# Optimization experiments

Measured on AMD Instinct MI355X. Metric: run time of the kernel, lower is better.

The kernel has to match this reference:

```python
import jax, jax.numpy as jnp
import numpy as np

D_MODEL = 1024
N_HEADS = 16
HEAD_DIM = D_MODEL // N_HEADS


def setup_inputs() -> dict:
    key = jax.random.key(0)
    k_x, k_qkv, k_proj = jax.random.split(key, 3)
    x = jax.random.normal(k_x, (2, 2048, D_MODEL), dtype=jnp.float32)
    # flax nnx.Linear kernels: shape (in_features, out_features), lecun_normal-ish scale
    w_qkv = jax.random.normal(k_qkv, (D_MODEL, 3 * D_MODEL), dtype=jnp.float32) / np.sqrt(D_MODEL)
    w_proj = jax.random.normal(k_proj, (D_MODEL, D_MODEL), dtype=jnp.float32) / np.sqrt(D_MODEL)
    return {"x": x, "w_qkv": w_qkv, "w_proj": w_proj}


def reference(x, w_qkv, w_proj):
    bsz, seq_len, d_model = x.shape
    qkv = x @ w_qkv  # (B, T, 3*D)
    q, k, v = jnp.split(qkv, 3, axis=-1)
    q = q.reshape(bsz, seq_len, N_HEADS, HEAD_DIM)
    k = k.reshape(bsz, seq_len, N_HEADS, HEAD_DIM)
    v = v.reshape(bsz, seq_len, N_HEADS, HEAD_DIM)
    scale = jnp.sqrt(jnp.asarray(HEAD_DIM, dtype=x.dtype))
    attn_logits = jnp.einsum('bthd,bshd->bhts', q / scale, k)  # (B, H, T, T)
    attn_weights = jax.nn.softmax(attn_logits, axis=-1)
    attn_out = jnp.einsum('bhts,bshd->bthd', attn_weights, v)
    attn_out = attn_out.reshape(bsz, seq_len, d_model)
    return attn_out @ w_proj
```

## Files before the change

kernel.cpp:

```cpp
#include <hip/hip_runtime.h>
#include <hip/hip_bf16.h>
#include <cmath>

#define D_MODEL 1024
#define NH 16
#define HD 64
#define BSZ 2
#define SEQ 2048
#define MTOT (BSZ * SEQ)

typedef _Float16 f16x8 __attribute__((ext_vector_type(8)));
typedef __fp16   fp16x2 __attribute__((ext_vector_type(2)));
typedef float    f32x4  __attribute__((ext_vector_type(4)));
typedef float    f32x16 __attribute__((ext_vector_type(16)));
typedef unsigned int uivec2 __attribute__((ext_vector_type(2)));

#define QSCALE 0.18033688011112042f

__device__ __forceinline__ ushort f2h(float x) {
    union { _Float16 h; ushort u; } cv;
    cv.h = (_Float16)x;
    return cv.u;
}
__device__ __forceinline__ uint pkh(float a, float b) {
    union { fp16x2 h; uint u; } cv;
    cv.h = __builtin_amdgcn_cvt_pkrtz(a, b);
    return cv.u;
}
__device__ __forceinline__ float fexp2(float x) {
    float r; asm("v_exp_f32 %0, %1" : "=v"(r) : "v"(x)); return r;
}
__device__ __forceinline__ float fmax3(float a, float b, float c) {
    return fmaxf(fmaxf(a, b), c);
}
__device__ __forceinline__ void gload_lds16(const ushort* g, ushort* l) {
    __builtin_amdgcn_global_load_lds(
        (const __attribute__((address_space(1))) void*)g,
        (__attribute__((address_space(3))) void*)l, 16, 0, 0);
}

__global__ __launch_bounds__(256)
void transpose_cast2(const float* __restrict__ A, const float* __restrict__ B,
                     ushort* __restrict__ At, ushort* __restrict__ Bt)
{
    __shared__ float tile[32][33];
    const int z = blockIdx.z;
    const float* in = (z < 3) ? A : B;
    ushort* out     = (z < 3) ? At : Bt;
    const int C     = (z < 3) ? 3 * D_MODEL : D_MODEL;
    const int cb    = (z < 3) ? z * 32 + blockIdx.x : blockIdx.x;
    const int R = D_MODEL;
    const int t  = threadIdx.x;
    const int r0 = blockIdx.y * 32, c0 = cb * 32;
    const int tr = t >> 5, tc = t & 31;
#pragma unroll
    for (int s = 0; s < 4; ++s)
        tile[tr + 8 * s][tc] = in[(size_t)(r0 + tr + 8 * s) * C + c0 + tc];
    __syncthreads();
#pragma unroll
    for (int s = 0; s < 4; ++s)
        out[(size_t)(c0 + tr + 8 * s) * R + r0 + tc] = f2h(tile[tc][tr + 8 * s]);
}

__global__ __launch_bounds__(256)
void gemm_qkv(const float* __restrict__ A, const ushort* __restrict__ Bt,
              ushort* __restrict__ Qw, ushort* __restrict__ Kw,
              ushort* __restrict__ Vw)
{
    __shared__ ushort As[3][128 * 32];
    __shared__ ushort Bs[3][128 * 32];

    const int t  = threadIdx.x;
    const int w  = t >> 6;
    const int l  = t & 63;
    const int lr = l & 15;
    const int lg = l >> 4;
    const int wr = w >> 1, wc = w & 1;

    const int gx   = gridDim.x;
    const int nwg  = gx * gridDim.y;
    const int lin  = blockIdx.y * gx + blockIdx.x;
    const int lin2 = (lin & 7) * (nwg >> 3) + (lin >> 3);
    const int m0   = (lin2 / gx) * 128;
    const int n0   = (lin2 % gx) * 128;

    const float*  Ab = A  + (size_t)m0 * 1024;
    const ushort* Bb = Bt + (size_t)n0 * 1024;

    f32x4 acc[4][4];
#pragma unroll
    for (int i = 0; i < 4; ++i)
#pragma unroll
        for (int j = 0; j < 4; ++j) acc[i][j] = (f32x4){0.f, 0.f, 0.f, 0.f};

    const int arow = w * 32 + (l >> 3);
    const int acol = (l & 7) * 4;
    float4 ar[4];
    auto loadA = [&](int kt) {
#pragma unroll
        for (int s = 0; s < 4; ++s)
            ar[s] = *(const float4*)(Ab + (size_t)(arow + s * 8) * 1024
                                        + kt * 32 + acol);
    };
    auto writeA = [&](int buf) {
#pragma unroll
        for (int s = 0; s < 4; ++s) {
            alignas(8) ushort e4[4];
            e4[0] = f2h(ar[s].x); e4[1] = f2h(ar[s].y);
            e4[2] = f2h(ar[s].z); e4[3] = f2h(ar[s].w);
            *(uint2*)&As[buf][(arow + s * 8) * 32 + acol] = *(const uint2*)e4;
        }
    };
    auto stageB = [&](int buf, int kt) {
#pragma unroll
        for (int s = 0; s < 2; ++s) {
            const int c    = s * 64 + l;
            const int row  = w * 32 + (c >> 2);
            const int unit = c & 3;
            gload_lds16(Bb + (size_t)row * 1024 + kt * 32 + unit * 8,
                        &Bs[buf][(w * 128 + s * 64) * 8]);
        }
    };

    auto body = [&](int kt, int cb, int vm) {
        if (vm == 2) asm volatile("s_waitcnt vmcnt(2)" ::: "memory");
        else         asm volatile("s_waitcnt vmcnt(0)" ::: "memory");
        asm volatile("s_waitcnt lgkmcnt(0)" ::: "memory");
        __builtin_amdgcn_s_barrier();

        if (kt + 1 < 32) writeA((cb + 1) % 3);
        if (kt + 2 < 32) { loadA(kt + 2); stageB((cb + 2) % 3, kt + 2); }

        f16x8 af[4], bf[4];
#pragma unroll
        for (int m = 0; m < 4; ++m)
            af[m] = *(const f16x8*)&As[cb][(wr * 64 + m * 16 + lr) * 32 + lg * 8];
#pragma unroll
        for (int n = 0; n < 4; ++n)
            bf[n] = *(const f16x8*)&Bs[cb][(wc * 64 + n * 16 + lr) * 32 + lg * 8];
        __builtin_amdgcn_s_setprio(1);
#pragma unroll
        for (int m = 0; m < 4; ++m)
#pragma unroll
            for (int n = 0; n < 4; ++n)
                acc[m][n] = __builtin_amdgcn_mfma_f32_16x16x32_f16(
                    af[m], bf[n], acc[m][n], 0, 0, 0);
        __builtin_amdgcn_s_setprio(0);
        __builtin_amdgcn_s_barrier();
    };

    loadA(0); stageB(0, 0);
    asm volatile("s_waitcnt vmcnt(2)" ::: "memory");
    writeA(0);
    loadA(1); stageB(1, 1);

#pragma unroll 1
    for (int i = 0; i < 10; ++i) {
        body(i * 3 + 0, 0, 2);
        body(i * 3 + 1, 1, 2);
        body(i * 3 + 2, 2, 2);
    }
    body(30, 0, 2);
    body(31, 1, 0);

#pragma unroll
    for (int mf = 0; mf < 4; ++mf) {
        const int row = m0 + wr * 64 + mf * 16 + lg * 4;
        const int b   = row >> 11;
        const int tt0 = row & (SEQ - 1);
#pragma unroll
        for (int nf = 0; nf < 4; ++nf) {
            const int col   = n0 + wc * 64 + nf * 16 + lr;
            const int which = col >> 10;
            const int h     = (col >> 6) & 15;
            const int d     = col & 63;
            if (which == 2) {
                ushort* p = Vw + (((size_t)(b * NH + h) * HD + d) * SEQ) + tt0;
                alignas(8) ushort e4[4];
#pragma unroll
                for (int i = 0; i < 4; ++i) e4[i] = f2h(acc[mf][nf][i]);
                *(uint2*)p = *(const uint2*)e4;
            } else {
                ushort* dst = (which == 0) ? Qw : Kw;
                const float sc = (which == 0) ? QSCALE : 1.0f;
#pragma unroll
                for (int i = 0; i < 4; ++i)
                    dst[((size_t)(b * NH + h) * SEQ + tt0 + i) * HD + d] =
                        f2h(acc[mf][nf][i] * sc);
            }
        }
    }
}

__global__ __launch_bounds__(256)
void gemm_proj(const ushort* __restrict__ A, const ushort* __restrict__ Bt,
               float* __restrict__ outp)
{
    __shared__ ushort As[3][128 * 32];
    __shared__ ushort Bs[3][128 * 32];

    const int t  = threadIdx.x;
    const int w  = t >> 6;
    const int l  = t & 63;
    const int lr = l & 15;
    const int lg = l >> 4;
    const int wr = w >> 1, wc = w & 1;

    const int gx   = gridDim.x;
    const int nwg  = gx * gridDim.y;
    const int lin  = blockIdx.y * gx + blockIdx.x;
    const int lin2 = (lin & 7) * (nwg >> 3) + (lin >> 3);
    const int m0   = (lin2 / gx) * 128;
    const int n0   = (lin2 % gx) * 128;

    const ushort* Ab = A  + (size_t)m0 * 1024;
    const ushort* Bb = Bt + (size_t)n0 * 1024;

    f32x4 acc[4][4];
#pragma unroll
    for (int i = 0; i < 4; ++i)
#pragma unroll
        for (int j = 0; j < 4; ++j) acc[i][j] = (f32x4){0.f, 0.f, 0.f, 0.f};

    auto stage = [&](int buf, int kt) {
        const int k0 = kt * 32;
#pragma unroll
        for (int s = 0; s < 2; ++s) {
            const int c    = s * 64 + l;
            const int row  = w * 32 + (c >> 2);
            const int unit = c & 3;
            gload_lds16(Ab + (size_t)row * 1024 + k0 + unit * 8,
                        &As[buf][(w * 128 + s * 64) * 8]);
            gload_lds16(Bb + (size_t)row * 1024 + k0 + unit * 8,
                        &Bs[buf][(w * 128 + s * 64) * 8]);
        }
    };

    auto body = [&](int kt, int cb, int vm) {
        if (kt + 2 < 32) stage((cb + 2) % 3, kt + 2);
        if (vm == 8)      asm volatile("s_waitcnt vmcnt(8)" ::: "memory");
        else if (vm == 4) asm volatile("s_waitcnt vmcnt(4)" ::: "memory");
        else              asm volatile("s_waitcnt vmcnt(0)" ::: "memory");
        __builtin_amdgcn_s_barrier();

        f16x8 af[4], bf[4];
#pragma unroll
        for (int m = 0; m < 4; ++m)
            af[m] = *(const f16x8*)&As[cb][(wr * 64 + m * 16 + lr) * 32 + lg * 8];
#pragma unroll
        for (int n = 0; n < 4; ++n)
            bf[n] = *(const f16x8*)&Bs[cb][(wc * 64 + n * 16 + lr) * 32 + lg * 8];
        __builtin_amdgcn_s_setprio(1);
#pragma unroll
        for (int m = 0; m < 4; ++m)
#pragma unroll
            for (int n = 0; n < 4; ++n)
                acc[m][n] = __builtin_amdgcn_mfma_f32_16x16x32_f16(
                    af[m], bf[n], acc[m][n], 0, 0, 0);
        __builtin_amdgcn_s_setprio(0);
        __builtin_amdgcn_s_barrier();
    };

    stage(0, 0);
    stage(1, 1);
#pragma unroll 1
    for (int i = 0; i < 10; ++i) {
        body(i * 3 + 0, 0, 8);
        body(i * 3 + 1, 1, 8);
        body(i * 3 + 2, 2, 8);
    }
    body(30, 0, 4);
    body(31, 1, 0);

#pragma unroll
    for (int mf = 0; mf < 4; ++mf) {
        const int row = m0 + wr * 64 + mf * 16 + lg * 4;
#pragma unroll
        for (int nf = 0; nf < 4; ++nf) {
            const int col = n0 + wc * 64 + nf * 16 + lr;
#pragma unroll
            for (int i = 0; i < 4; ++i)
                outp[(size_t)(row + i) * 1024 + col] = acc[mf][nf][i];
        }
    }
}

__global__ __launch_bounds__(512, 4)
void attn_mfma7(const ushort* __restrict__ Qw, const ushort* __restrict__ Kw,
                const ushort* __restrict__ Vtg, ushort* __restrict__ AO)
{
    __shared__ ushort KsAll[2][2][64 * 64];
    __shared__ ushort VtAll[2][2][64 * 64];

    const int t    = threadIdx.x;
    const int w    = t >> 6;
    const int l    = t & 63;
    const int q    = l & 31;
    const int hi   = l >> 5;
    const int half = w >> 2;
    const int ww   = w & 3;

    const int bh = blockIdx.y;
    const int q0 = blockIdx.x * 128 + ww * 32;
    const int kbase = half * (SEQ / 2);
    const int NT = (SEQ / 2) / 64;

    const ushort* Qp = Qw  + (size_t)bh * SEQ * HD;
    const ushort* Kp = Kw  + (size_t)bh * SEQ * HD;
    const ushort* Vp = Vtg + (size_t)bh * HD * SEQ;

    ushort (*Ks)[64 * 64] = KsAll[half];
    ushort (*Vt)[64 * 64] = VtAll[half];

    f16x8 qf[4];
#pragma unroll
    for (int kc = 0; kc < 4; ++kc)
        qf[kc] = *(const f16x8*)(Qp + (size_t)(q0 + q) * HD + kc * 16 + hi * 8);

    f32x16 oacc[2];
#pragma unroll
    for (int db = 0; db < 2; ++db)
#pragma unroll
        for (int r = 0; r < 16; ++r) oacc[db][r] = 0.f;
    float m_run = -3.0e38f, l_run = 0.f;

    auto stageK = [&](int buf, int k0) {
#pragma unroll
        for (int s = 0; s < 2; ++s) {
            const int c    = ww * 64 + l + 256 * s;
            const int row  = c >> 3;
            const int unit = (c & 7) ^ (row & 7);
            gload_lds16(Kp + (size_t)(k0 + row) * HD + unit * 8,
                        &Ks[buf][(ww * 64 + 256 * s) * 8]);
        }
    };
    auto stageV = [&](int buf, int k0) {
#pragma unroll
        for (int s = 0; s < 2; ++s) {
            const int c    = ww * 64 + l + 256 * s;
            const int row  = c >> 3;
            const int unit = (c & 7) ^ (row & 7);
            gload_lds16(Vp + (size_t)row * SEQ + k0 + unit * 8,
                        &Vt[buf][(ww * 64 + 256 * s) * 8]);
        }
    };

    stageK(0, kbase);
    stageV(0, kbase);
    __syncthreads();

    int cur = 0;
    for (int kt = 0; kt < NT; ++kt) {
        if (kt + 1 < NT) {
            stageK(cur ^ 1, kbase + (kt + 1) * 64);
            stageV(cur ^ 1, kbase + (kt + 1) * 64);
        }

        f32x16 sacc[2];
        __builtin_amdgcn_s_setprio(1);
#pragma unroll
        for (int kb = 0; kb < 2; ++kb) {
            f32x16 a;
#pragma unroll
            for (int r = 0; r < 16; ++r) a[r] = 0.f;
            const int row = kb * 32 + q;
            const int swz = (row & 7) << 4;
#pragma unroll
            for (int kc = 0; kc < 4; ++kc) {
                f16x8 kf = *(const f16x8*)(
                    (const char*)Ks[cur] + row * 128 + ((kc * 32 + hi * 16) ^ swz));
                a = __builtin_amdgcn_mfma_f32_32x32x16_f16(kf, qf[kc], a, 0, 0, 0);
            }
            sacc[kb] = a;
        }
        __builtin_amdgcn_s_setprio(0);

        float p0 = fmax3(fmaxf(sacc[0][0], sacc[1][0]),
                         fmaxf(sacc[0][1], sacc[1][1]),
                         fmaxf(sacc[0][2], sacc[1][2]));
        float p1 = fmax3(fmaxf(sacc[0][3], sacc[1][3]),
                         fmaxf(sacc[0][4], sacc[1][4]),
                         fmaxf(sacc[0][5], sacc[1][5]));
        float p2 = fmax3(fmaxf(sacc[0][6], sacc[1][6]),
                         fmaxf(sacc[0][7], sacc[1][7]),
                         fmaxf(sacc[0][8], sacc[1][8]));
        float p3 = fmax3(fmaxf(sacc[0][9], sacc[1][9]),
                         fmaxf(sacc[0][10], sacc[1][10]),
                         fmaxf(sacc[0][11], sacc[1][11]));
        float p4 = fmax3(fmaxf(sacc[0][12], sacc[1][12]),
                         fmaxf(sacc[0][13], sacc[1][13]),
                         fmaxf(sacc[0][14], sacc[1][14]));
        float p5 = fmaxf(sacc[0][15], sacc[1][15]);
        float mx = fmaxf(fmax3(p0, p1, p2), fmax3(p3, p4, p5));
        mx = fmaxf(mx, __shfl_xor(mx, 32));

        if (__any(mx > m_run + 8.0f)) {
            const float m_new = fmaxf(m_run, mx);
            const float scale = fexp2(m_run - m_new);
            m_run = m_new;
            l_run *= scale;
#pragma unroll
            for (int db = 0; db < 2; ++db)
#pragma unroll
                for (int r = 0; r < 16; ++r) oacc[db][r] *= scale;
        }

#pragma unroll
        for (int kb = 0; kb < 2; ++kb)
#pragma unroll
            for (int r = 0; r < 16; ++r)
                sacc[kb][r] = fexp2(sacc[kb][r] - m_run);

        float ts[16];
#pragma unroll
        for (int r = 0; r < 16; ++r) ts[r] = sacc[0][r] + sacc[1][r];
#pragma unroll
        for (int s = 8; s > 0; s >>= 1)
#pragma unroll
            for (int r = 0; r < 8; ++r)
                if (r < s) ts[r] += ts[r + s];
        l_run += ts[0] + __shfl_xor(ts[0], 32);

        f16x8 pfrag[4];
#pragma unroll
        for (int kb = 0; kb < 2; ++kb)
#pragma unroll
            for (int lc = 0; lc < 2; ++lc) {
                const int rb = lc * 8;
                uint a = pkh(sacc[kb][rb + 0], sacc[kb][rb + 1]);
                uint b = pkh(sacc[kb][rb + 2], sacc[kb][rb + 3]);
                uint c = pkh(sacc[kb][rb + 4], sacc[kb][rb + 5]);
                uint d = pkh(sacc[kb][rb + 6], sacc[kb][rb + 7]);
                uivec2 r0 = __builtin_amdgcn_permlane32_swap(a, c, false, false);
                uivec2 r1 = __builtin_amdgcn_permlane32_swap(b, d, false, false);
                union { uint u[4]; f16x8 v; } f;
                f.u[0] = r0.x;
                f.u[1] = r1.x;
                f.u[2] = r0.y;
                f.u[3] = r1.y;
                pfrag[kb * 2 + lc] = f.v;
            }

        __builtin_amdgcn_s_setprio(1);
#pragma unroll
        for (int db = 0; db < 2; ++db) {
            const int row = db * 32 + q;
            const int swz = (row & 7) << 4;
#pragma unroll
            for (int kc = 0; kc < 4; ++kc) {
                f16x8 vf = *(const f16x8*)(
                    (const char*)Vt[cur] + row * 128 + ((kc * 32 + hi * 16) ^ swz));
                oacc[db] = __builtin_amdgcn_mfma_f32_32x32x16_f16(
                    vf, pfrag[kc], oacc[db], 0, 0, 0);
            }
        }
        __builtin_amdgcn_s_setprio(0);

        __syncthreads();
        cur ^= 1;
    }

    float* oex = (float*)KsAll;
    float* mex = (float*)VtAll;
    float* lex = mex + 256;

    if (half == 1) {
        mex[ww * 64 + l] = m_run;
        lex[ww * 64 + l] = l_run;
#pragma unroll
        for (int db = 0; db < 2; ++db)
#pragma unroll
            for (int r = 0; r < 16; ++r)
                oex[(((ww * 2 + db) * 16) + r) * 64 + l] = oacc[db][r];
    }
    __syncthreads();
    if (half == 0) {
        const float m2 = mex[ww * 64 + l];
        const float l2 = lex[ww * 64 + l];
        const float mf = fmaxf(m_run, m2);
        float w1 = fexp2(m_run - mf), w2 = fexp2(m2 - mf);
        const float inv = 1.f / (l_run * w1 + l2 * w2);
        w1 *= inv; w2 *= inv;

        const int b = bh >> 4, h = bh & 15;
        ushort* orow = AO + ((size_t)(b * SEQ) + q0 + q) * D_MODEL + h * HD;
#pragma unroll
        for (int db = 0; db < 2; ++db)
#pragma unroll
            for (int g = 0; g < 4; ++g) {
                const int d = db * 32 + g * 8 + hi * 4;
                alignas(8) ushort e4[4];
#pragma unroll
                for (int i = 0; i < 4; ++i) {
                    const float o2 = oex[(((ww * 2 + db) * 16) + g * 4 + i) * 64 + l];
                    e4[i] = f2h(oacc[db][g * 4 + i] * w1 + o2 * w2);
                }
                *(uint2*)(orow + d) = *(const uint2*)e4;
            }
    }
}

extern "C" void kernel_launch(void* const* d_in, const int* in_sizes, int n_in,
                              void* d_out, int out_size, void* d_ws, size_t ws_size,
                              hipStream_t stream)
{
    const float* x      = (const float*)d_in[0];
    const float* w_qkv  = (const float*)d_in[1];
    const float* w_proj = (const float*)d_in[2];
    float* out = (float*)d_out;

    ushort* WqT = (ushort*)d_ws;
    ushort* WpT = WqT + (size_t)3 * D_MODEL * D_MODEL;
    ushort* Qw  = WpT + (size_t)D_MODEL * D_MODEL;
    ushort* Kw  = Qw  + (size_t)MTOT * D_MODEL;
    ushort* Vt  = Kw  + (size_t)MTOT * D_MODEL;
    ushort* AOh = Vt  + (size_t)MTOT * D_MODEL;

    dim3 blk(256);

    transpose_cast2<<<dim3(32, 32, 4), blk, 0, stream>>>(w_qkv, w_proj, WqT, WpT);

    gemm_qkv<<<dim3(3 * D_MODEL / 128, MTOT / 128), blk, 0, stream>>>(
        x, WqT, Qw, Kw, Vt);

    attn_mfma7<<<dim3(SEQ / 128, BSZ * NH), dim3(512), 0, stream>>>(Qw, Kw, Vt, AOh);

    gemm_proj<<<dim3(D_MODEL / 128, MTOT / 128), blk, 0, stream>>>(AOh, WpT, out);
}
```

Before: 142.5 us.

## Stage fp32 A via direct-to-LDS loads in QKV GEMM, remap block order

```diff
diff --git a/kernel.cpp b/kernel.cpp
--- a/kernel.cpp
+++ b/kernel.cpp
@@ -33,25 +33,23 @@
 __device__ __forceinline__ float fmax3(float a, float b, float c) {
     return fmaxf(fmaxf(a, b), c);
 }
-__device__ __forceinline__ void gload_lds16(const ushort* g, ushort* l) {
+__device__ __forceinline__ void gload_lds16(const void* g, void* l) {
     __builtin_amdgcn_global_load_lds(
         (const __attribute__((address_space(1))) void*)g,
         (__attribute__((address_space(3))) void*)l, 16, 0, 0);
 }
 
 __global__ __launch_bounds__(256)
-void transpose_cast2(const float* __restrict__ A, const float* __restrict__ B,
-                     ushort* __restrict__ At, ushort* __restrict__ Bt)
+void prep_w(const float* __restrict__ Wq, const float* __restrict__ Wp,
+            ushort* __restrict__ WqT, ushort* __restrict__ WpT)
 {
     __shared__ float tile[32][33];
-    const int z = blockIdx.z;
-    const float* in = (z < 3) ? A : B;
-    ushort* out     = (z < 3) ? At : Bt;
-    const int C     = (z < 3) ? 3 * D_MODEL : D_MODEL;
-    const int cb    = (z < 3) ? z * 32 + blockIdx.x : blockIdx.x;
-    const int R = D_MODEL;
+    const int b = blockIdx.x;
+    const float* in; ushort* out; int C, cb, rb;
+    if (b < 3072) { in = Wq; out = WqT; C = 3 * D_MODEL; cb = b % 96; rb = b / 96; }
+    else { const int b2 = b - 3072; in = Wp; out = WpT; C = D_MODEL; cb = b2 & 31; rb = b2 >> 5; }
     const int t  = threadIdx.x;
-    const int r0 = blockIdx.y * 32, c0 = cb * 32;
+    const int r0 = rb * 32, c0 = cb * 32;
     const int tr = t >> 5, tc = t & 31;
 #pragma unroll
     for (int s = 0; s < 4; ++s)
@@ -59,15 +57,15 @@
     __syncthreads();
 #pragma unroll
     for (int s = 0; s < 4; ++s)
-        out[(size_t)(c0 + tr + 8 * s) * R + r0 + tc] = f2h(tile[tc][tr + 8 * s]);
+        out[(size_t)(c0 + tr + 8 * s) * D_MODEL + r0 + tc] = f2h(tile[tc][tr + 8 * s]);
 }
 
 __global__ __launch_bounds__(256)
-void gemm_qkv(const float* __restrict__ A, const ushort* __restrict__ Bt,
-              ushort* __restrict__ Qw, ushort* __restrict__ Kw,
-              ushort* __restrict__ Vw)
+void gemm_qkv32(const float* __restrict__ A, const ushort* __restrict__ Bt,
+                ushort* __restrict__ Qw, ushort* __restrict__ Kw,
+                ushort* __restrict__ Vw)
 {
-    __shared__ ushort As[3][128 * 32];
+    __shared__ float  Asf[2][128 * 32];
     __shared__ ushort Bs[3][128 * 32];
 
     const int t  = threadIdx.x;
@@ -77,12 +75,12 @@
     const int lg = l >> 4;
     const int wr = w >> 1, wc = w & 1;
 
-    const int gx   = gridDim.x;
-    const int nwg  = gx * gridDim.y;
-    const int lin  = blockIdx.y * gx + blockIdx.x;
-    const int lin2 = (lin & 7) * (nwg >> 3) + (lin >> 3);
-    const int m0   = (lin2 / gx) * 128;
-    const int n0   = (lin2 % gx) * 128;
+    const int nb  = gridDim.x, mb = gridDim.y;
+    const int lin = blockIdx.y * nb + blockIdx.x;
+    const int per = (nb * mb) >> 3;
+    const int id2 = (lin & 7) * per + (lin >> 3);
+    const int n0  = (id2 / mb) * 128;
+    const int m0  = (id2 % mb) * 128;
 
     const float*  Ab = A  + (size_t)m0 * 1024;
     const ushort* Bb = Bt + (size_t)n0 * 1024;
@@ -93,22 +91,15 @@
 #pragma unroll
         for (int j = 0; j < 4; ++j) acc[i][j] = (f32x4){0.f, 0.f, 0.f, 0.f};
 
-    const int arow = w * 32 + (l >> 3);
-    const int acol = (l & 7) * 4;
-    float4 ar[4];
-    auto loadA = [&](int kt) {
-#pragma unroll
-        for (int s = 0; s < 4; ++s)
-            ar[s] = *(const float4*)(Ab + (size_t)(arow + s * 8) * 1024
-                                        + kt * 32 + acol);
-    };
-    auto writeA = [&](int buf) {
+    auto stageA = [&](int buf, int kt) {
 #pragma unroll
         for (int s = 0; s < 4; ++s) {
-            alignas(8) ushort e4[4];
-            e4[0] = f2h(ar[s].x); e4[1] = f2h(ar[s].y);
-            e4[2] = f2h(ar[s].z); e4[3] = f2h(ar[s].w);
-            *(uint2*)&As[buf][(arow + s * 8) * 32 + acol] = *(const uint2*)e4;
+            const int c   = w * 256 + s * 64 + l;
+            const int row = c >> 3;
+            const int g   = c & 7;
+            const int src = (((g >> 1) ^ (row & 3)) << 3) + ((g & 1) << 2);
+            gload_lds16(Ab + (size_t)row * 1024 + kt * 32 + src,
+                        &Asf[buf][(w * 256 + s * 64) * 4]);
         }
     };
     auto stageB = [&](int buf, int kt) {
@@ -122,22 +113,33 @@
         }
     };
 
-    auto body = [&](int kt, int cb, int vm) {
-        if (vm == 2) asm volatile("s_waitcnt vmcnt(2)" ::: "memory");
-        else         asm volatile("s_waitcnt vmcnt(0)" ::: "memory");
-        asm volatile("s_waitcnt lgkmcnt(0)" ::: "memory");
+    auto body = [&](int kt, int ab, int bb, int vm, bool doA, bool doB) {
+        if (vm == 6)      asm volatile("s_waitcnt vmcnt(6)" ::: "memory");
+        else if (vm == 2) asm volatile("s_waitcnt vmcnt(2)" ::: "memory");
+        else              asm volatile("s_waitcnt vmcnt(0)" ::: "memory");
         __builtin_amdgcn_s_barrier();
 
-        if (kt + 1 < 32) writeA((cb + 1) % 3);
-        if (kt + 2 < 32) { loadA(kt + 2); stageB((cb + 2) % 3, kt + 2); }
+        if (doA) stageA(ab ^ 1, kt + 1);
+        if (doB) stageB((bb + 2) % 3, kt + 2);
 
         f16x8 af[4], bf[4];
 #pragma unroll
-        for (int m = 0; m < 4; ++m)
-            af[m] = *(const f16x8*)&As[cb][(wr * 64 + m * 16 + lr) * 32 + lg * 8];
+        for (int m = 0; m < 4; ++m) {
+            const int row = wr * 64 + m * 16 + lr;
+            const char* p = (const char*)&Asf[ab][0]
+                          + row * 128 + ((lg ^ (row & 3)) << 5);
+            f32x4 v0 = *(const f32x4*)p;
+            f32x4 v1 = *(const f32x4*)(p + 16);
+            union { uint u[4]; f16x8 v; } cv;
+            cv.u[0] = pkh(v0[0], v0[1]);
+            cv.u[1] = pkh(v0[2], v0[3]);
+            cv.u[2] = pkh(v1[0], v1[1]);
+            cv.u[3] = pkh(v1[2], v1[3]);
+            af[m] = cv.v;
+        }
 #pragma unroll
         for (int n = 0; n < 4; ++n)
-            bf[n] = *(const f16x8*)&Bs[cb][(wc * 64 + n * 16 + lr) * 32 + lg * 8];
+            bf[n] = *(const f16x8*)&Bs[bb][(wc * 64 + n * 16 + lr) * 32 + lg * 8];
         __builtin_amdgcn_s_setprio(1);
 #pragma unroll
         for (int m = 0; m < 4; ++m)
@@ -146,22 +148,21 @@
                 acc[m][n] = __builtin_amdgcn_mfma_f32_16x16x32_f16(
                     af[m], bf[n], acc[m][n], 0, 0, 0);
         __builtin_amdgcn_s_setprio(0);
-        __builtin_amdgcn_s_barrier();
-    };
-
-    loadA(0); stageB(0, 0);
-    asm volatile("s_waitcnt vmcnt(2)" ::: "memory");
-    writeA(0);
-    loadA(1); stageB(1, 1);
-
+    };
+
+    stageA(0, 0); stageB(0, 0);
+    stageA(1, 1); stageB(1, 1);
+
+    body(0, 0, 0, 6, false, true);
 #pragma unroll 1
-    for (int i = 0; i < 10; ++i) {
-        body(i * 3 + 0, 0, 2);
-        body(i * 3 + 1, 1, 2);
-        body(i * 3 + 2, 2, 2);
-    }
-    body(30, 0, 2);
-    body(31, 1, 0);
+    for (int i = 0; i < 5; ++i) {
+#pragma unroll
+        for (int j = 1; j <= 6; ++j) {
+            const int kt = i * 6 + j;
+            body(kt, kt & 1, kt % 3, 2, true, kt + 2 < 32);
+        }
+    }
+    body(31, 1, 1, 0, false, false);
 
 #pragma unroll
     for (int mf = 0; mf < 4; ++mf) {
@@ -206,12 +207,12 @@
     const int lg = l >> 4;
     const int wr = w >> 1, wc = w & 1;
 
-    const int gx   = gridDim.x;
-    const int nwg  = gx * gridDim.y;
-    const int lin  = blockIdx.y * gx + blockIdx.x;
-    const int lin2 = (lin & 7) * (nwg >> 3) + (lin >> 3);
-    const int m0   = (lin2 / gx) * 128;
-    const int n0   = (lin2 % gx) * 128;
+    const int nb  = gridDim.x, mb = gridDim.y;
+    const int lin = blockIdx.y * nb + blockIdx.x;
+    const int per = (nb * mb) >> 3;
+    const int id2 = (lin & 7) * per + (lin >> 3);
+    const int n0  = (id2 / mb) * 128;
+    const int m0  = (id2 % mb) * 128;
 
     const ushort* Ab = A  + (size_t)m0 * 1024;
     const ushort* Bb = Bt + (size_t)n0 * 1024;
@@ -286,7 +287,7 @@
 }
 
 __global__ __launch_bounds__(512, 4)
-void attn_mfma7(const ushort* __restrict__ Qw, const ushort* __restrict__ Kw,
+void attn_mfma8(const ushort* __restrict__ Qw, const ushort* __restrict__ Kw,
                 const ushort* __restrict__ Vtg, ushort* __restrict__ AO)
 {
     __shared__ ushort KsAll[2][2][64 * 64];
@@ -300,8 +301,11 @@
     const int half = w >> 2;
     const int ww   = w & 3;
 
-    const int bh = blockIdx.y;
-    const int q0 = blockIdx.x * 128 + ww * 32;
+    const int lin = blockIdx.y * 16 + blockIdx.x;
+    const int id2 = (lin & 7) * 64 + (lin >> 3);
+    const int bh  = id2 >> 4;
+    const int q0  = (id2 & 15) * 128 + ww * 32;
+
     const int kbase = half * (SEQ / 2);
     const int NT = (SEQ / 2) / 64;
 
@@ -323,6 +327,10 @@
 #pragma unroll
         for (int r = 0; r < 16; ++r) oacc[db][r] = 0.f;
     float m_run = -3.0e38f, l_run = 0.f;
+
+    f32x16 z16;
+#pragma unroll
+    for (int r = 0; r < 16; ++r) z16[r] = 0.f;
 
     auto stageK = [&](int buf, int k0) {
 #pragma unroll
@@ -360,13 +368,13 @@
         __builtin_amdgcn_s_setprio(1);
 #pragma unroll
         for (int kb = 0; kb < 2; ++kb) {
-            f32x16 a;
-#pragma unroll
-            for (int r = 0; r < 16; ++r) a[r] = 0.f;
             const int row = kb * 32 + q;
             const int swz = (row & 7) << 4;
-#pragma unroll
-            for (int kc = 0; kc < 4; ++kc) {
+            f16x8 kf0 = *(const f16x8*)(
+                (const char*)Ks[cur] + row * 128 + ((hi * 16) ^ swz));
+            f32x16 a = __builtin_amdgcn_mfma_f32_32x32x16_f16(kf0, qf[0], z16, 0, 0, 0);
+#pragma unroll
+            for (int kc = 1; kc < 4; ++kc) {
                 f16x8 kf = *(const f16x8*)(
                     (const char*)Ks[cur] + row * 128 + ((kc * 32 + hi * 16) ^ swz));
                 a = __builtin_amdgcn_mfma_f32_32x32x16_f16(kf, qf[kc], a, 0, 0, 0);
@@ -518,12 +526,12 @@
 
     dim3 blk(256);
 
-    transpose_cast2<<<dim3(32, 32, 4), blk, 0, stream>>>(w_qkv, w_proj, WqT, WpT);
-
-    gemm_qkv<<<dim3(3 * D_MODEL / 128, MTOT / 128), blk, 0, stream>>>(
+    prep_w<<<dim3(3072 + 1024), blk, 0, stream>>>(w_qkv, w_proj, WqT, WpT);
+
+    gemm_qkv32<<<dim3(3 * D_MODEL / 128, MTOT / 128), blk, 0, stream>>>(
         x, WqT, Qw, Kw, Vt);
 
-    attn_mfma7<<<dim3(SEQ / 128, BSZ * NH), dim3(512), 0, stream>>>(Qw, Kw, Vt, AOh);
+    attn_mfma8<<<dim3(SEQ / 128, BSZ * NH), dim3(512), 0, stream>>>(Qw, Kw, Vt, AOh);
 
     gemm_proj<<<dim3(D_MODEL / 128, MTOT / 128), blk, 0, stream>>>(AOh, WpT, out);
 }
```

Result: slower. 145.4 us (+2.0%).
